# Performance work log

Measured on AMD Instinct MI355X. Metric: run time of the kernel, lower is better.

The kernel has to match this reference:

```python
import jax, jax.numpy as jnp
import numpy as np

NUM_USERS = 100000
NUM_ITEMS = 100000
N = NUM_USERS + NUM_ITEMS
D = 64
E = 3200000


def setup_inputs() -> dict:
    key = jax.random.key(0)
    ks = jax.random.split(key, 8)
    edge_index = jax.random.randint(ks[0], (2, E), 0, N, dtype=jnp.int64)
    edge_weight = jax.random.uniform(ks[1], (E,), dtype=jnp.float32)
    user_emb = jax.random.normal(ks[2], (NUM_USERS, D), dtype=jnp.float32) * 0.1
    item_emb = jax.random.normal(ks[3], (NUM_ITEMS, D), dtype=jnp.float32) * 0.1
    s = 1.0 / np.sqrt(D)
    W1 = jax.random.uniform(ks[4], (D, D), dtype=jnp.float32, minval=-s, maxval=s)
    b1 = jax.random.uniform(ks[5], (D,), dtype=jnp.float32, minval=-s, maxval=s)
    W2 = jax.random.uniform(ks[6], (D, D), dtype=jnp.float32, minval=-s, maxval=s)
    b2 = jax.random.uniform(ks[7], (D,), dtype=jnp.float32, minval=-s, maxval=s)
    return {"edge_index": edge_index, "edge_weight": edge_weight,
            "user_emb": user_emb, "item_emb": item_emb,
            "W1": W1, "b1": b1, "W2": W2, "b2": b2}


def _gcn_layer(x, src, dst, edge_weight, W, b):
    # message: edge_weight * x[src]; aggregate: scatter-add at dst
    msg = edge_weight[:, None] * x[src]              # [E, D] gather + mul
    agg = jax.ops.segment_sum(msg, dst, num_segments=N)  # [N, D] scatter-add
    updated = (agg + x) * 0.5                        # residual average
    return updated @ W + b                           # linear


def reference(edge_index, edge_weight, user_emb, item_emb, W1, b1, W2, b2):
    src = edge_index[0]
    dst = edge_index[1]
    x = jnp.concatenate([user_emb, item_emb], axis=0)  # [N, D]
    x = _gcn_layer(x, src, dst, edge_weight, W1, b1)
    x = _gcn_layer(x, src, dst, edge_weight, W2, b2)
    return x
```

## Files before the change

### kernel.cpp

```cpp
#include <hip/hip_runtime.h>
#include <hip/hip_fp16.h>

#define NUM_USERS 100000
#define NN        200000
#define DD        64
#define EE        3200000

#define KB_   391
#define GSEG  512
#define EPS   (EE / GSEG)
#define CVX_BLOCKS 12500
#define CVW_BLOCKS 32

typedef _Float16 half8 __attribute__((ext_vector_type(8)));
typedef _Float16 half4 __attribute__((ext_vector_type(4)));
typedef float    f32x4 __attribute__((ext_vector_type(4)));

__global__ __launch_bounds__(256) void prep_kernel(
    const int* __restrict__ ei,
    const float* __restrict__ xu, const float* __restrict__ xi,
    const float* __restrict__ W1, const float* __restrict__ W2,
    int* __restrict__ counts_seg, _Float16* __restrict__ xh,
    _Float16* __restrict__ Wt)
{
    __shared__ int h[KB_];
    const int b = blockIdx.x;
    const int t = threadIdx.x;
    if (b < GSEG) {
        for (int k = t; k < KB_; k += 256) h[k] = 0;
        __syncthreads();
        const int base = b * EPS;
        for (int i = t; i < EPS; i += 256) {
            const int dst = ei[EE + base + i];
            atomicAdd(&h[dst >> 9], 1);
        }
        __syncthreads();
        for (int k = t; k < KB_; k += 256)
            counts_seg[b * KB_ + k] = h[k];
    } else if (b < GSEG + CVX_BLOCKS) {
        const int i = (b - GSEG) * 256 + t;
        const float4 v = (i < NUM_USERS * DD / 4)
                           ? ((const float4*)xu)[i]
                           : ((const float4*)xi)[i - NUM_USERS * DD / 4];
        half4 o; o[0] = (_Float16)v.x; o[1] = (_Float16)v.y;
                 o[2] = (_Float16)v.z; o[3] = (_Float16)v.w;
        ((half4*)xh)[i] = o;
    } else {
        const int idx = (b - GSEG - CVX_BLOCKS) * 256 + t;
        const int mat = idx >> 12, rem = idx & 4095, k = rem >> 6, n = rem & 63;
        const float* W = mat ? W2 : W1;
        Wt[mat * DD * DD + n * DD + k] = (_Float16)W[k * DD + n];
    }
}

__global__ __launch_bounds__(256) void bscan_kernel(
    int* __restrict__ counts_seg, int* __restrict__ btot)
{
    __shared__ int part[256];
    const int k = blockIdx.x;
    const int t = threadIdx.x;
    const int c0 = counts_seg[(2 * t)     * KB_ + k];
    const int c1 = counts_seg[(2 * t + 1) * KB_ + k];
    const int run = c0 + c1;
    part[t] = run; __syncthreads();
    for (int off = 1; off < 256; off <<= 1) {
        int add = (t >= off) ? part[t - off] : 0;
        __syncthreads();
        part[t] += add;
        __syncthreads();
    }
    const int base = part[t] - run;
    counts_seg[(2 * t)     * KB_ + k] = base;
    counts_seg[(2 * t + 1) * KB_ + k] = base + c0;
    if (t == 255) btot[k] = part[255];
}

__global__ __launch_bounds__(256) void append_kernel(
    const int* __restrict__ ei, const float* __restrict__ ew,
    const int* __restrict__ counts_seg, const int* __restrict__ btot,
    int2* __restrict__ etmp)
{
    __shared__ int sb[512];
    __shared__ int part[256];
    __shared__ int fr[KB_];
    const int s = blockIdx.x;
    const int t = threadIdx.x;
    for (int j = t; j < 512; j += 256) sb[j] = (j < KB_) ? btot[j] : 0;
    __syncthreads();
    {
        const int c0 = sb[2 * t], c1 = sb[2 * t + 1];
        const int run = c0 + c1;
        part[t] = run; __syncthreads();
        for (int off = 1; off < 256; off <<= 1) {
            int add = (t >= off) ? part[t - off] : 0;
            __syncthreads();
            part[t] += add;
            __syncthreads();
        }
        const int base = part[t] - run;
        sb[2 * t]     = base;
        sb[2 * t + 1] = base + c0;
    }
    __syncthreads();
    for (int k = t; k < KB_; k += 256)
        fr[k] = sb[k] + counts_seg[s * KB_ + k];
    __syncthreads();
    const int base = s * EPS;
    for (int i = t; i < EPS; i += 256) {
        const int e   = base + i;
        const int   src = ei[e];
        const int   dst = ei[EE + e];
        const float w   = ew[e];
        const int k  = dst >> 9;
        const int dl = dst & 511;
        const int pos = atomicAdd(&fr[k], 1);
        etmp[pos] = make_int2(src | (dl << 18), __float_as_int(w));
    }
}

__global__ __launch_bounds__(256) void place_kernel(
    const int2* __restrict__ etmp, const int* __restrict__ btot,
    int2* __restrict__ edges, int* __restrict__ row_ptr)
{
    __shared__ int sb[512];
    __shared__ int part[256];
    __shared__ int cnt[512];
    __shared__ int cur[512];
    const int k = blockIdx.x;
    const int t = threadIdx.x;
    for (int j = t; j < 512; j += 256) sb[j] = (j < KB_) ? btot[j] : 0;
    __syncthreads();
    {
        const int c0 = sb[2 * t], c1 = sb[2 * t + 1];
        const int run = c0 + c1;
        part[t] = run; __syncthreads();
        for (int off = 1; off < 256; off <<= 1) {
            int add = (t >= off) ? part[t - off] : 0;
            __syncthreads();
            part[t] += add;
            __syncthreads();
        }
        const int base = part[t] - run;
        sb[2 * t]     = base;
        sb[2 * t + 1] = base + c0;
    }
    __syncthreads();
    const int beg = sb[k];
    const int end = (k == KB_ - 1) ? EE : sb[k + 1];
    cnt[t] = 0; cnt[t + 256] = 0;
    __syncthreads();
    for (int e = beg + t; e < end; e += 256)
        atomicAdd(&cnt[((unsigned)etmp[e].x) >> 18], 1);
    __syncthreads();
    const int c0 = cnt[2 * t], c1 = cnt[2 * t + 1];
    const int run = c0 + c1;
    part[t] = run; __syncthreads();
    for (int off = 1; off < 256; off <<= 1) {
        int add = (t >= off) ? part[t - off] : 0;
        __syncthreads();
        part[t] += add;
        __syncthreads();
    }
    const int base = beg + part[t] - run;
    cur[2 * t]     = base;
    cur[2 * t + 1] = base + c0;
    const int node0 = (k << 9) + 2 * t;
    if (node0 < NN)     row_ptr[node0]     = base;
    if (node0 + 1 < NN) row_ptr[node0 + 1] = base + c0;
    if (k == KB_ - 1 && t == 0) row_ptr[NN] = EE;
    __syncthreads();
    for (int e = beg + t; e < end; e += 256) {
        const int2 r  = etmp[e];
        const int  dl = ((unsigned)r.x) >> 18;
        const int  pos = atomicAdd(&cur[dl], 1);
        edges[pos] = make_int2((r.x & 0x3FFFF) << 7, r.y);
    }
}

__global__ __launch_bounds__(256) void aggregate_kernel(
    const int2* __restrict__ edges, const int* __restrict__ row_ptr,
    const _Float16* __restrict__ xh, _Float16* __restrict__ u)
{
    const int wave = (blockIdx.x * 256 + threadIdx.x) >> 6;
    const int lane = threadIdx.x & 63;
    const unsigned lane2 = lane * 2;
    const int nbase = wave * 4;
    const char* xb = (const char*)xh;

    int bnd[5];
#pragma unroll
    for (int k = 0; k < 5; ++k)
        bnd[k] = __builtin_amdgcn_readfirstlane(row_ptr[nbase + k]);

    float acc[4];
#pragma unroll
    for (int k = 0; k < 4; ++k)
        acc[k] = (float)*(const _Float16*)(xb + ((unsigned)(nbase + k) << 7) + lane2);

    int e0 = bnd[0], e1 = bnd[1], e2 = bnd[2], e3 = bnd[3];
    const int f0 = bnd[1], f1 = bnd[2], f2 = bnd[3], f3 = bnd[4];

    while ((e0 + 4 <= f0) && (e1 + 4 <= f1) && (e2 + 4 <= f2) && (e3 + 4 <= f3)) {
        const int2 a0 = edges[e0 + 0], a1 = edges[e0 + 1];
        const int2 a2 = edges[e0 + 2], a3 = edges[e0 + 3];
        const int2 b0 = edges[e1 + 0], b1 = edges[e1 + 1];
        const int2 b2 = edges[e1 + 2], b3 = edges[e1 + 3];
        const int2 c0 = edges[e2 + 0], c1 = edges[e2 + 1];
        const int2 c2 = edges[e2 + 2], c3 = edges[e2 + 3];
        const int2 d0 = edges[e3 + 0], d1 = edges[e3 + 1];
        const int2 d2 = edges[e3 + 2], d3 = edges[e3 + 3];

        const float va0 = (float)*(const _Float16*)(xb + (unsigned)a0.x + lane2);
        const float va1 = (float)*(const _Float16*)(xb + (unsigned)a1.x + lane2);
        const float va2 = (float)*(const _Float16*)(xb + (unsigned)a2.x + lane2);
        const float va3 = (float)*(const _Float16*)(xb + (unsigned)a3.x + lane2);
        const float vb0 = (float)*(const _Float16*)(xb + (unsigned)b0.x + lane2);
        const float vb1 = (float)*(const _Float16*)(xb + (unsigned)b1.x + lane2);
        const float vb2 = (float)*(const _Float16*)(xb + (unsigned)b2.x + lane2);
        const float vb3 = (float)*(const _Float16*)(xb + (unsigned)b3.x + lane2);
        const float vc0 = (float)*(const _Float16*)(xb + (unsigned)c0.x + lane2);
        const float vc1 = (float)*(const _Float16*)(xb + (unsigned)c1.x + lane2);
        const float vc2 = (float)*(const _Float16*)(xb + (unsigned)c2.x + lane2);
        const float vc3 = (float)*(const _Float16*)(xb + (unsigned)c3.x + lane2);
        const float vd0 = (float)*(const _Float16*)(xb + (unsigned)d0.x + lane2);
        const float vd1 = (float)*(const _Float16*)(xb + (unsigned)d1.x + lane2);
        const float vd2 = (float)*(const _Float16*)(xb + (unsigned)d2.x + lane2);
        const float vd3 = (float)*(const _Float16*)(xb + (unsigned)d3.x + lane2);

        acc[0] = fmaf(__int_as_float(a0.y), va0, acc[0]);
        acc[0] = fmaf(__int_as_float(a1.y), va1, acc[0]);
        acc[0] = fmaf(__int_as_float(a2.y), va2, acc[0]);
        acc[0] = fmaf(__int_as_float(a3.y), va3, acc[0]);
        acc[1] = fmaf(__int_as_float(b0.y), vb0, acc[1]);
        acc[1] = fmaf(__int_as_float(b1.y), vb1, acc[1]);
        acc[1] = fmaf(__int_as_float(b2.y), vb2, acc[1]);
        acc[1] = fmaf(__int_as_float(b3.y), vb3, acc[1]);
        acc[2] = fmaf(__int_as_float(c0.y), vc0, acc[2]);
        acc[2] = fmaf(__int_as_float(c1.y), vc1, acc[2]);
        acc[2] = fmaf(__int_as_float(c2.y), vc2, acc[2]);
        acc[2] = fmaf(__int_as_float(c3.y), vc3, acc[2]);
        acc[3] = fmaf(__int_as_float(d0.y), vd0, acc[3]);
        acc[3] = fmaf(__int_as_float(d1.y), vd1, acc[3]);
        acc[3] = fmaf(__int_as_float(d2.y), vd2, acc[3]);
        acc[3] = fmaf(__int_as_float(d3.y), vd3, acc[3]);

        e0 += 4; e1 += 4; e2 += 4; e3 += 4;
    }

    {
        int e = e0;
        for (; e + 4 <= f0; e += 4) {
            const int2 r0 = edges[e + 0], r1 = edges[e + 1];
            const int2 r2 = edges[e + 2], r3 = edges[e + 3];
            const float v0 = (float)*(const _Float16*)(xb + (unsigned)r0.x + lane2);
            const float v1 = (float)*(const _Float16*)(xb + (unsigned)r1.x + lane2);
            const float v2 = (float)*(const _Float16*)(xb + (unsigned)r2.x + lane2);
            const float v3 = (float)*(const _Float16*)(xb + (unsigned)r3.x + lane2);
            acc[0] = fmaf(__int_as_float(r0.y), v0, acc[0]);
            acc[0] = fmaf(__int_as_float(r1.y), v1, acc[0]);
            acc[0] = fmaf(__int_as_float(r2.y), v2, acc[0]);
            acc[0] = fmaf(__int_as_float(r3.y), v3, acc[0]);
        }
        for (; e < f0; ++e) {
            const int2 p = edges[e];
            acc[0] = fmaf(__int_as_float(p.y),
                          (float)*(const _Float16*)(xb + (unsigned)p.x + lane2), acc[0]);
        }
    }
    {
        int e = e1;
        for (; e + 4 <= f1; e += 4) {
            const int2 r0 = edges[e + 0], r1 = edges[e + 1];
            const int2 r2 = edges[e + 2], r3 = edges[e + 3];
            const float v0 = (float)*(const _Float16*)(xb + (unsigned)r0.x + lane2);
            const float v1 = (float)*(const _Float16*)(xb + (unsigned)r1.x + lane2);
            const float v2 = (float)*(const _Float16*)(xb + (unsigned)r2.x + lane2);
            const float v3 = (float)*(const _Float16*)(xb + (unsigned)r3.x + lane2);
            acc[1] = fmaf(__int_as_float(r0.y), v0, acc[1]);
            acc[1] = fmaf(__int_as_float(r1.y), v1, acc[1]);
            acc[1] = fmaf(__int_as_float(r2.y), v2, acc[1]);
            acc[1] = fmaf(__int_as_float(r3.y), v3, acc[1]);
        }
        for (; e < f1; ++e) {
            const int2 p = edges[e];
            acc[1] = fmaf(__int_as_float(p.y),
                          (float)*(const _Float16*)(xb + (unsigned)p.x + lane2), acc[1]);
        }
    }
    {
        int e = e2;
        for (; e + 4 <= f2; e += 4) {
            const int2 r0 = edges[e + 0], r1 = edges[e + 1];
            const int2 r2 = edges[e + 2], r3 = edges[e + 3];
            const float v0 = (float)*(const _Float16*)(xb + (unsigned)r0.x + lane2);
            const float v1 = (float)*(const _Float16*)(xb + (unsigned)r1.x + lane2);
            const float v2 = (float)*(const _Float16*)(xb + (unsigned)r2.x + lane2);
            const float v3 = (float)*(const _Float16*)(xb + (unsigned)r3.x + lane2);
            acc[2] = fmaf(__int_as_float(r0.y), v0, acc[2]);
            acc[2] = fmaf(__int_as_float(r1.y), v1, acc[2]);
            acc[2] = fmaf(__int_as_float(r2.y), v2, acc[2]);
            acc[2] = fmaf(__int_as_float(r3.y), v3, acc[2]);
        }
        for (; e < f2; ++e) {
            const int2 p = edges[e];
            acc[2] = fmaf(__int_as_float(p.y),
                          (float)*(const _Float16*)(xb + (unsigned)p.x + lane2), acc[2]);
        }
    }
    {
        int e = e3;
        for (; e + 4 <= f3; e += 4) {
            const int2 r0 = edges[e + 0], r1 = edges[e + 1];
            const int2 r2 = edges[e + 2], r3 = edges[e + 3];
            const float v0 = (float)*(const _Float16*)(xb + (unsigned)r0.x + lane2);
            const float v1 = (float)*(const _Float16*)(xb + (unsigned)r1.x + lane2);
            const float v2 = (float)*(const _Float16*)(xb + (unsigned)r2.x + lane2);
            const float v3 = (float)*(const _Float16*)(xb + (unsigned)r3.x + lane2);
            acc[3] = fmaf(__int_as_float(r0.y), v0, acc[3]);
            acc[3] = fmaf(__int_as_float(r1.y), v1, acc[3]);
            acc[3] = fmaf(__int_as_float(r2.y), v2, acc[3]);
            acc[3] = fmaf(__int_as_float(r3.y), v3, acc[3]);
        }
        for (; e < f3; ++e) {
            const int2 p = edges[e];
            acc[3] = fmaf(__int_as_float(p.y),
                          (float)*(const _Float16*)(xb + (unsigned)p.x + lane2), acc[3]);
        }
    }

    char* ub = (char*)u;
#pragma unroll
    for (int k = 0; k < 4; ++k)
        *(_Float16*)(ub + ((unsigned)(nbase + k) << 7) + lane2) = (_Float16)(acc[k] * 0.5f);
}

template<bool HALF_OUT>
__global__ __launch_bounds__(256) void gemm64_kernel(
    const _Float16* __restrict__ u, const _Float16* __restrict__ Wt,
    const float* __restrict__ bias, void* __restrict__ outp)
{
    const int wid  = blockIdx.x * 4 + (threadIdx.x >> 6);
    const int lane = threadIdx.x & 63;
    const int m    = lane & 15;
    const int quad = lane >> 4;
    const size_t rowbase = (size_t)wid * 16;

    half8 bf[4][2];
#pragma unroll
    for (int c = 0; c < 4; ++c)
#pragma unroll
        for (int h = 0; h < 2; ++h)
            bf[c][h] = *(const half8*)(Wt + (size_t)(c * 16 + m) * DD + h * 32 + quad * 8);

    const half8 a0 = *(const half8*)(u + (rowbase + m) * DD +  0 + quad * 8);
    const half8 a1 = *(const half8*)(u + (rowbase + m) * DD + 32 + quad * 8);

    f32x4 acc[4];
#pragma unroll
    for (int c = 0; c < 4; ++c) {
        f32x4 z = {0.f, 0.f, 0.f, 0.f};
        z = __builtin_amdgcn_mfma_f32_16x16x32_f16(a0, bf[c][0], z, 0, 0, 0);
        z = __builtin_amdgcn_mfma_f32_16x16x32_f16(a1, bf[c][1], z, 0, 0, 0);
        acc[c] = z;
    }

#pragma unroll
    for (int c = 0; c < 4; ++c) {
        const float bv = bias[c * 16 + m];
#pragma unroll
        for (int r = 0; r < 4; ++r) {
            const size_t row = rowbase + quad * 4 + r;
            const float val = acc[c][r] + bv;
            if (HALF_OUT) ((_Float16*)outp)[row * DD + c * 16 + m] = (_Float16)val;
            else          ((float*)    outp)[row * DD + c * 16 + m] = val;
        }
    }
}

extern "C" void kernel_launch(void* const* d_in, const int* in_sizes, int n_in,
                              void* d_out, int out_size, void* d_ws, size_t ws_size,
                              hipStream_t stream) {
    const int*   edge_index  = (const int*)  d_in[0];
    const float* edge_weight = (const float*)d_in[1];
    const float* user_emb    = (const float*)d_in[2];
    const float* item_emb    = (const float*)d_in[3];
    const float* W1          = (const float*)d_in[4];
    const float* b1          = (const float*)d_in[5];
    const float* W2          = (const float*)d_in[6];
    const float* b2          = (const float*)d_in[7];
    float*       out         = (float*)d_out;

    char* ws = (char*)d_ws;
    _Float16* xh        = (_Float16*)(ws);
    _Float16* u         = (_Float16*)(ws + 25600000);
    int2*     etmp      = (int2*)    (ws + 25600000);
    int2*     edges     = (int2*)    (ws + 51200000);
    int*      row_ptr   = (int*)     (ws + 76800000);
    int*      counts_seg= (int*)     (ws + 77600064);
    int*      btot      = (int*)     (ws + 78400832);
    _Float16* Wt        = (_Float16*)(ws + 78402432);

    const int gemm_blocks = (NN / 16) / 4;
    const int agg_blocks  = NN / 16;
    const int prep_blocks = GSEG + CVX_BLOCKS + CVW_BLOCKS;

    prep_kernel  <<<prep_blocks, 256, 0, stream>>>(edge_index, user_emb, item_emb,
                                                   W1, W2, counts_seg, xh, Wt);
    bscan_kernel <<<KB_,  256, 0, stream>>>(counts_seg, btot);
    append_kernel<<<GSEG, 256, 0, stream>>>(edge_index, edge_weight,
                                            counts_seg, btot, etmp);
    place_kernel <<<KB_,  256, 0, stream>>>(etmp, btot, edges, row_ptr);

    aggregate_kernel<<<agg_blocks, 256, 0, stream>>>(edges, row_ptr, xh, u);
    gemm64_kernel<true><<<gemm_blocks, 256, 0, stream>>>(u, Wt, b1, (void*)xh);

    aggregate_kernel<<<agg_blocks, 256, 0, stream>>>(edges, row_ptr, xh, u);
    gemm64_kernel<false><<<gemm_blocks, 256, 0, stream>>>(u, Wt + DD * DD, b2, (void*)out);
}
```

Baseline: 430.9 us.

## Fuse neighbor aggregation with the 64x64 MFMA linear layer

Merges the aggregate kernel and the GEMM kernel into a single kernel. Each block aggregates 16 nodes, stages them in LDS, and each wave runs one 16-column MFMA slice before writing the biased output. This removes the round trip of the intermediate u buffer through global memory and two kernel launches. The cost is a block-wide barrier between the gather and GEMM phases, and the layer-1 output now goes to a separate buffer (the etmp region) instead of overwriting xh.

```diff
diff --git a/kernel.cpp b/kernel.cpp
--- a/kernel.cpp
+++ b/kernel.cpp
@@ -177,14 +177,18 @@
     }
 }
 
-__global__ __launch_bounds__(256) void aggregate_kernel(
+template<bool HALF_OUT>
+__global__ __launch_bounds__(256) void agg_gemm_kernel(
     const int2* __restrict__ edges, const int* __restrict__ row_ptr,
-    const _Float16* __restrict__ xh, _Float16* __restrict__ u)
-{
-    const int wave = (blockIdx.x * 256 + threadIdx.x) >> 6;
-    const int lane = threadIdx.x & 63;
+    const _Float16* __restrict__ xh, const _Float16* __restrict__ Wt,
+    const float* __restrict__ bias, void* __restrict__ outp)
+{
+    __shared__ _Float16 ut[16][72];
+    const int t    = threadIdx.x;
+    const int w    = t >> 6;
+    const int lane = t & 63;
     const unsigned lane2 = lane * 2;
-    const int nbase = wave * 4;
+    const int nbase = blockIdx.x * 16 + w * 4;
     const char* xb = (const char*)xh;
 
     int bnd[5];
@@ -328,52 +332,28 @@
         }
     }
 
-    char* ub = (char*)u;
 #pragma unroll
     for (int k = 0; k < 4; ++k)
-        *(_Float16*)(ub + ((unsigned)(nbase + k) << 7) + lane2) = (_Float16)(acc[k] * 0.5f);
-}
-
-template<bool HALF_OUT>
-__global__ __launch_bounds__(256) void gemm64_kernel(
-    const _Float16* __restrict__ u, const _Float16* __restrict__ Wt,
-    const float* __restrict__ bias, void* __restrict__ outp)
-{
-    const int wid  = blockIdx.x * 4 + (threadIdx.x >> 6);
-    const int lane = threadIdx.x & 63;
+        ut[(w << 2) + k][lane] = (_Float16)(acc[k] * 0.5f);
+    __syncthreads();
+
     const int m    = lane & 15;
     const int quad = lane >> 4;
-    const size_t rowbase = (size_t)wid * 16;
-
-    half8 bf[4][2];
+    const half8 a0 = *(const half8*)(&ut[m][ 0 + quad * 8]);
+    const half8 a1 = *(const half8*)(&ut[m][32 + quad * 8]);
+    const half8 w0 = *(const half8*)(Wt + (size_t)(w * 16 + m) * DD +  0 + quad * 8);
+    const half8 w1 = *(const half8*)(Wt + (size_t)(w * 16 + m) * DD + 32 + quad * 8);
+    f32x4 z = {0.f, 0.f, 0.f, 0.f};
+    z = __builtin_amdgcn_mfma_f32_16x16x32_f16(a0, w0, z, 0, 0, 0);
+    z = __builtin_amdgcn_mfma_f32_16x16x32_f16(a1, w1, z, 0, 0, 0);
+    const float bv = bias[w * 16 + m];
+    const int rowb = blockIdx.x * 16;
 #pragma unroll
-    for (int c = 0; c < 4; ++c)
-#pragma unroll
-        for (int h = 0; h < 2; ++h)
-            bf[c][h] = *(const half8*)(Wt + (size_t)(c * 16 + m) * DD + h * 32 + quad * 8);
-
-    const half8 a0 = *(const half8*)(u + (rowbase + m) * DD +  0 + quad * 8);
-    const half8 a1 = *(const half8*)(u + (rowbase + m) * DD + 32 + quad * 8);
-
-    f32x4 acc[4];
-#pragma unroll
-    for (int c = 0; c < 4; ++c) {
-        f32x4 z = {0.f, 0.f, 0.f, 0.f};
-        z = __builtin_amdgcn_mfma_f32_16x16x32_f16(a0, bf[c][0], z, 0, 0, 0);
-        z = __builtin_amdgcn_mfma_f32_16x16x32_f16(a1, bf[c][1], z, 0, 0, 0);
-        acc[c] = z;
-    }
-
-#pragma unroll
-    for (int c = 0; c < 4; ++c) {
-        const float bv = bias[c * 16 + m];
-#pragma unroll
-        for (int r = 0; r < 4; ++r) {
-            const size_t row = rowbase + quad * 4 + r;
-            const float val = acc[c][r] + bv;
-            if (HALF_OUT) ((_Float16*)outp)[row * DD + c * 16 + m] = (_Float16)val;
-            else          ((float*)    outp)[row * DD + c * 16 + m] = val;
-        }
+    for (int r = 0; r < 4; ++r) {
+        const int row = rowb + quad * 4 + r;
+        const float val = z[r] + bv;
+        if (HALF_OUT) ((_Float16*)outp)[row * DD + w * 16 + m] = (_Float16)val;
+        else          ((float*)    outp)[row * DD + w * 16 + m] = val;
     }
 }
 
@@ -392,7 +372,7 @@
 
     char* ws = (char*)d_ws;
     _Float16* xh        = (_Float16*)(ws);
-    _Float16* u         = (_Float16*)(ws + 25600000);
+    _Float16* uh        = (_Float16*)(ws + 25600000);
     int2*     etmp      = (int2*)    (ws + 25600000);
     int2*     edges     = (int2*)    (ws + 51200000);
     int*      row_ptr   = (int*)     (ws + 76800000);
@@ -400,7 +380,6 @@
     int*      btot      = (int*)     (ws + 78400832);
     _Float16* Wt        = (_Float16*)(ws + 78402432);
 
-    const int gemm_blocks = (NN / 16) / 4;
     const int agg_blocks  = NN / 16;
     const int prep_blocks = GSEG + CVX_BLOCKS + CVW_BLOCKS;
 
@@ -411,9 +390,8 @@
                                             counts_seg, btot, etmp);
     place_kernel <<<KB_,  256, 0, stream>>>(etmp, btot, edges, row_ptr);
 
-    aggregate_kernel<<<agg_blocks, 256, 0, stream>>>(edges, row_ptr, xh, u);
-    gemm64_kernel<true><<<gemm_blocks, 256, 0, stream>>>(u, Wt, b1, (void*)xh);
-
-    aggregate_kernel<<<agg_blocks, 256, 0, stream>>>(edges, row_ptr, xh, u);
-    gemm64_kernel<false><<<gemm_blocks, 256, 0, stream>>>(u, Wt + DD * DD, b2, (void*)out);
-}
+    agg_gemm_kernel<true ><<<agg_blocks, 256, 0, stream>>>(edges, row_ptr, xh,
+                                                           Wt, b1, (void*)uh);
+    agg_gemm_kernel<false><<<agg_blocks, 256, 0, stream>>>(edges, row_ptr, uh,
+                                                           Wt + DD * DD, b2, (void*)out);
+}
```

After: 416.0 us. 1.04x faster.
